# Kernel tuning notes

Measured on AMD Instinct MI355X. Metric: run time of the kernel, lower is better.

## Reference

```python
import jax, jax.numpy as jnp
import numpy as np

M, IN, H, OUT = 64, 3, 256, 3
B = 8192
W0_FIRST = 30.0
W0_HIDDEN = 30.0


def setup_inputs() -> dict:
    key = jax.random.key(0)
    ks = jax.random.split(key, 12)
    fb = 1.0 / IN                                   # first-layer bound
    hb = np.sqrt(6.0 / H) / W0_HIDDEN               # hidden bound
    x = jax.random.uniform(ks[0], (B, IN), jnp.float32, -1.0, 1.0)
    w0 = jax.random.uniform(ks[1], (M, H, IN), jnp.float32, -fb, fb)
    b0 = jnp.zeros((M, H), jnp.float32)
    w1 = jax.random.uniform(ks[2], (M, H, H), jnp.float32, -hb, hb)
    b1 = jnp.zeros((M, H), jnp.float32)
    w2 = jax.random.uniform(ks[3], (M, H, H), jnp.float32, -hb, hb)
    b2 = jnp.zeros((M, H), jnp.float32)
    w3 = jax.random.uniform(ks[4], (M, H, H), jnp.float32, -hb, hb)
    b3 = jnp.zeros((M, H), jnp.float32)
    wf = jax.random.uniform(ks[5], (M, OUT, H), jnp.float32, -hb, hb)
    bf = jnp.zeros((M, OUT), jnp.float32)
    return {"x": x, "w0": w0, "b0": b0, "w1": w1, "b1": b1,
            "w2": w2, "b2": b2, "w3": w3, "b3": b3, "wf": wf, "bf": bf}


def reference(x, w0, b0, w1, b1, w2, b2, w3, b3, wf, bf):
    # first sine layer: [B,in] x [M,H,in] -> [B,M,H]
    h = jnp.sin(W0_FIRST * (jnp.einsum('bi,moi->bmo', x, w0) + b0[None]))
    # hidden sine layers
    for w, b in ((w1, b1), (w2, b2), (w3, b3)):
        h = jnp.sin(W0_HIDDEN * (jnp.einsum('bmi,moi->bmo', h, w) + b[None]))
    # final linear: [B,M,H] x [M,out,H] -> [B,M,out]
    return jnp.einsum('bmi,moi->bmo', h, wf) + bf[None]
```

## Files before the change

kernel.cpp:

```cpp
#include <hip/hip_runtime.h>

#define BATCH 8192
#define MEXP  64
#define HDIM  256
#define INDIM 3
#define ODIM  3
#define BT    64
#define SINSC 4.774648292756860f

typedef __attribute__((ext_vector_type(8))) _Float16 f16x8;
typedef __attribute__((ext_vector_type(4))) float    f32x4;

__device__ __forceinline__ int swz(int row, int byteInRow) {
  return (row * 512 + byteInRow) ^ (((row ^ (row >> 3)) & 7) << 4);
}

__global__ void prep_hidden(const float* __restrict__ w1, const float* __restrict__ w2,
                            const float* __restrict__ w3, _Float16* __restrict__ ws) {
  int chunk = blockIdx.x * 256 + threadIdx.x;
  int lm    = chunk >> 13;
  int c     = chunk & 8191;
  int layer = lm >> 6, m = lm & 63;
  int lane  = c & 63;
  int ctks  = c >> 6;
  int ct = ctks >> 3, ks = ctks & 7;
  int col = ct * 16 + (lane & 15);
  int k   = ks * 32 + ((lane >> 4) << 3);
  const float* w = (layer == 0) ? w1 : (layer == 1) ? w2 : w3;
  const float* src = w + ((size_t)m * HDIM + col) * HDIM + k;
  f16x8 v;
#pragma unroll
  for (int j = 0; j < 8; ++j) v[j] = (_Float16)src[j];
  *(f16x8*)(ws + (size_t)chunk * 8) = v;
}

__global__ void prep_wf(const float* __restrict__ wf, _Float16* __restrict__ ws) {
  int chunk = blockIdx.x * 256 + threadIdx.x;
  int m    = chunk >> 9;
  int c    = chunk & 511;
  int lane = c & 63;
  int ks   = c >> 6;
  int col  = lane & 15;
  int k    = ks * 32 + ((lane >> 4) << 3);
  f16x8 v;
  if (col < ODIM) {
    const float* src = wf + ((size_t)m * ODIM + col) * HDIM + k;
#pragma unroll
    for (int j = 0; j < 8; ++j) v[j] = (_Float16)src[j];
  } else {
#pragma unroll
    for (int j = 0; j < 8; ++j) v[j] = (_Float16)0.0f;
  }
  *(f16x8*)(ws + (size_t)chunk * 8) = v;
}

__device__ __forceinline__ void hidden_layer(char* hb, const _Float16* __restrict__ wl,
                                             const float* __restrict__ bptr, int w, int lane) {
  f32x4 acc[4][4] = {};
#pragma unroll
  for (int ks = 0; ks < 8; ++ks) {
    f16x8 a[4];
    f16x8 bb[4];
#pragma unroll
    for (int rt = 0; rt < 4; ++rt) {
      int row = rt * 16 + (lane & 15);
      a[rt] = *(const f16x8*)(hb + swz(row, ks * 64 + ((lane >> 4) << 4)));
    }
#pragma unroll
    for (int ct = 0; ct < 4; ++ct) {
      int chunk = ((w * 4 + ct) * 8 + ks) * 64 + lane;
      bb[ct] = *(const f16x8*)(wl + chunk * 8);
    }
#pragma unroll
    for (int rt = 0; rt < 4; ++rt)
#pragma unroll
      for (int ct = 0; ct < 4; ++ct)
        acc[rt][ct] = __builtin_amdgcn_mfma_f32_16x16x32_f16(a[rt], bb[ct], acc[rt][ct], 0, 0, 0);
  }
  __syncthreads();
#pragma unroll
  for (int ct = 0; ct < 4; ++ct) {
    int col = w * 64 + ct * 16 + (lane & 15);
    float bias = bptr[col];
#pragma unroll
    for (int rt = 0; rt < 4; ++rt) {
#pragma unroll
      for (int t = 0; t < 4; ++t) {
        int row = rt * 16 + ((lane >> 4) << 2) + t;
        float h = __builtin_amdgcn_sinf((acc[rt][ct][t] + bias) * SINSC);
        *(_Float16*)(hb + swz(row, col * 2)) = (_Float16)h;
      }
    }
  }
  __syncthreads();
}

__global__ __launch_bounds__(256, 2)
void siren_fused(const float* __restrict__ x, const float* __restrict__ w0,
                 const float* __restrict__ b0, const float* __restrict__ b1,
                 const float* __restrict__ b2, const float* __restrict__ b3,
                 const float* __restrict__ bfin, const _Float16* __restrict__ wh,
                 const _Float16* __restrict__ wff, float* __restrict__ out) {
  __shared__ _Float16 hbuf[BT * HDIM];
  char* hb = (char*)hbuf;

  int tid  = threadIdx.x;
  int lane = tid & 63;
  int w    = tid >> 6;
  int id   = blockIdx.x;
  int m    = ((id & 7) << 3) + ((id >> 3) >> 7);
  int tile = (id >> 3) & 127;

  {
    int col = tid;
    const float* wp = w0 + ((size_t)m * HDIM + col) * INDIM;
    float wc0 = wp[0], wc1 = wp[1], wc2 = wp[2];
    float bc  = b0[m * HDIM + col];
    const float* xp = x + (size_t)tile * BT * INDIM;
#pragma unroll 4
    for (int r = 0; r < BT; ++r) {
      float z = fmaf(xp[r * 3 + 2], wc2, fmaf(xp[r * 3 + 1], wc1, fmaf(xp[r * 3], wc0, bc)));
      float h = __builtin_amdgcn_sinf(z * SINSC);
      *(_Float16*)(hb + swz(r, col * 2)) = (_Float16)h;
    }
  }
  __syncthreads();

  hidden_layer(hb, wh + ((size_t)0 * MEXP + m) * (HDIM * HDIM), b1 + m * HDIM, w, lane);
  hidden_layer(hb, wh + ((size_t)1 * MEXP + m) * (HDIM * HDIM), b2 + m * HDIM, w, lane);
  hidden_layer(hb, wh + ((size_t)2 * MEXP + m) * (HDIM * HDIM), b3 + m * HDIM, w, lane);

  {
    f32x4 facc = {};
    const _Float16* wfp = wff + (size_t)m * (16 * HDIM);
#pragma unroll
    for (int ks = 0; ks < 8; ++ks) {
      int row = w * 16 + (lane & 15);
      f16x8 a   = *(const f16x8*)(hb + swz(row, ks * 64 + ((lane >> 4) << 4)));
      f16x8 bfr = *(const f16x8*)(wfp + ((size_t)(ks * 64 + lane)) * 8);
      facc = __builtin_amdgcn_mfma_f32_16x16x32_f16(a, bfr, facc, 0, 0, 0);
    }
    int col = lane & 15;
    if (col < ODIM) {
      float bv = bfin[m * ODIM + col];
#pragma unroll
      for (int t = 0; t < 4; ++t) {
        int row = w * 16 + ((lane >> 4) << 2) + t;
        int b   = tile * BT + row;
        out[((size_t)b * MEXP + m) * ODIM + col] = facc[t] + bv;
      }
    }
  }
}

extern "C" void kernel_launch(void* const* d_in, const int* in_sizes, int n_in,
                              void* d_out, int out_size, void* d_ws, size_t ws_size,
                              hipStream_t stream) {
  (void)in_sizes; (void)n_in; (void)out_size; (void)ws_size;
  const float* x  = (const float*)d_in[0];
  const float* w0 = (const float*)d_in[1];
  const float* b0 = (const float*)d_in[2];
  const float* w1 = (const float*)d_in[3];
  const float* b1 = (const float*)d_in[4];
  const float* w2 = (const float*)d_in[5];
  const float* b2 = (const float*)d_in[6];
  const float* w3 = (const float*)d_in[7];
  const float* b3 = (const float*)d_in[8];
  const float* wf = (const float*)d_in[9];
  const float* bf = (const float*)d_in[10];

  _Float16* wh  = (_Float16*)d_ws;
  _Float16* wff = wh + (size_t)3 * MEXP * HDIM * HDIM;

  prep_hidden<<<6144, 256, 0, stream>>>(w1, w2, w3, wh);
  prep_wf<<<128, 256, 0, stream>>>(wf, wff);
  siren_fused<<<8192, 256, 0, stream>>>(x, w0, b0, b1, b2, b3, bf, wh, wff, (float*)d_out);
}
```

Measured before the change: 397.7 us.

## Double batch tile to 128 rows with 8 waves and swapped MFMA operands

The batch tile grows from 64 to 128 rows and each block runs 512 threads, so every block reads each expert's hidden weights for twice as many rows. Each wave now owns 32 output columns across all 8 row tiles, keeps the weight fragments in registers with a one-step prefetch, and reads activations from LDS as the B operand. The transposed accumulator layout lets each lane write four results to LDS as one vector store. The sine scale is folded into the fp16 weights during preprocessing, and the bias is applied with an fma. LDS per block doubles to 64 KB and launch bounds change to 512 threads with 4 blocks per CU, which may limit occupancy.

```diff
diff --git a/kernel.cpp b/kernel.cpp
--- a/kernel.cpp
+++ b/kernel.cpp
@@ -1,14 +1,15 @@
 #include <hip/hip_runtime.h>
 
-#define BATCH 8192
 #define MEXP  64
 #define HDIM  256
 #define INDIM 3
 #define ODIM  3
-#define BT    64
+#define BT    128
+#define NTILE 64
 #define SINSC 4.774648292756860f
 
 typedef __attribute__((ext_vector_type(8))) _Float16 f16x8;
+typedef __attribute__((ext_vector_type(4))) _Float16 f16x4;
 typedef __attribute__((ext_vector_type(4))) float    f32x4;
 
 __device__ __forceinline__ int swz(int row, int byteInRow) {
@@ -30,7 +31,7 @@
   const float* src = w + ((size_t)m * HDIM + col) * HDIM + k;
   f16x8 v;
 #pragma unroll
-  for (int j = 0; j < 8; ++j) v[j] = (_Float16)src[j];
+  for (int j = 0; j < 8; ++j) v[j] = (_Float16)(src[j] * SINSC);
   *(f16x8*)(ws + (size_t)chunk * 8) = v;
 }
 
@@ -55,47 +56,45 @@
 }
 
 __device__ __forceinline__ void hidden_layer(char* hb, const _Float16* __restrict__ wl,
-                                             const float* __restrict__ bptr, int w, int lane) {
-  f32x4 acc[4][4] = {};
+                                             const float* __restrict__ bptr,
+                                             int wid, int lane, int g) {
+  f32x4 acc[8][2] = {};
+  const f16x8* wfrag = (const f16x8*)wl;
+  int ct0 = wid * 2, ct1 = ct0 + 1;
+  f16x8 A0 = wfrag[(ct0 * 8 + 0) * 64 + lane];
+  f16x8 A1 = wfrag[(ct1 * 8 + 0) * 64 + lane];
 #pragma unroll
   for (int ks = 0; ks < 8; ++ks) {
-    f16x8 a[4];
-    f16x8 bb[4];
-#pragma unroll
-    for (int rt = 0; rt < 4; ++rt) {
-      int row = rt * 16 + (lane & 15);
-      a[rt] = *(const f16x8*)(hb + swz(row, ks * 64 + ((lane >> 4) << 4)));
+    f16x8 a0 = A0, a1 = A1;
+    if (ks < 7) {
+      A0 = wfrag[(ct0 * 8 + ks + 1) * 64 + lane];
+      A1 = wfrag[(ct1 * 8 + ks + 1) * 64 + lane];
     }
 #pragma unroll
-    for (int ct = 0; ct < 4; ++ct) {
-      int chunk = ((w * 4 + ct) * 8 + ks) * 64 + lane;
-      bb[ct] = *(const f16x8*)(wl + chunk * 8);
+    for (int rt = 0; rt < 8; ++rt) {
+      f16x8 b = *(const f16x8*)(hb + swz(rt * 16 + (lane & 15), ks * 64 + g * 16));
+      acc[rt][0] = __builtin_amdgcn_mfma_f32_16x16x32_f16(a0, b, acc[rt][0], 0, 0, 0);
+      acc[rt][1] = __builtin_amdgcn_mfma_f32_16x16x32_f16(a1, b, acc[rt][1], 0, 0, 0);
     }
-#pragma unroll
-    for (int rt = 0; rt < 4; ++rt)
-#pragma unroll
-      for (int ct = 0; ct < 4; ++ct)
-        acc[rt][ct] = __builtin_amdgcn_mfma_f32_16x16x32_f16(a[rt], bb[ct], acc[rt][ct], 0, 0, 0);
   }
   __syncthreads();
 #pragma unroll
-  for (int ct = 0; ct < 4; ++ct) {
-    int col = w * 64 + ct * 16 + (lane & 15);
-    float bias = bptr[col];
+  for (int ct = 0; ct < 2; ++ct) {
+    int c0 = wid * 32 + ct * 16 + g * 4;
+    f32x4 bias = *(const f32x4*)(bptr + c0);
 #pragma unroll
-    for (int rt = 0; rt < 4; ++rt) {
+    for (int rt = 0; rt < 8; ++rt) {
+      f16x4 v;
 #pragma unroll
-      for (int t = 0; t < 4; ++t) {
-        int row = rt * 16 + ((lane >> 4) << 2) + t;
-        float h = __builtin_amdgcn_sinf((acc[rt][ct][t] + bias) * SINSC);
-        *(_Float16*)(hb + swz(row, col * 2)) = (_Float16)h;
-      }
+      for (int t = 0; t < 4; ++t)
+        v[t] = (_Float16)__builtin_amdgcn_sinf(fmaf(bias[t], SINSC, acc[rt][ct][t]));
+      *(f16x4*)(hb + swz(rt * 16 + (lane & 15), c0 * 2)) = v;
     }
   }
   __syncthreads();
 }
 
-__global__ __launch_bounds__(256, 2)
+__global__ __launch_bounds__(512, 4)
 void siren_fused(const float* __restrict__ x, const float* __restrict__ w0,
                  const float* __restrict__ b0, const float* __restrict__ b1,
                  const float* __restrict__ b2, const float* __restrict__ b3,
@@ -106,49 +105,46 @@
 
   int tid  = threadIdx.x;
   int lane = tid & 63;
-  int w    = tid >> 6;
+  int wid  = tid >> 6;
+  int g    = lane >> 4;
   int id   = blockIdx.x;
-  int m    = ((id & 7) << 3) + ((id >> 3) >> 7);
-  int tile = (id >> 3) & 127;
+  int m    = ((id & 7) << 3) + ((id >> 3) >> 6);
+  int tile = (id >> 3) & (NTILE - 1);
 
   {
-    int col = tid;
+    int col  = tid & 255;
+    int half = tid >> 8;
     const float* wp = w0 + ((size_t)m * HDIM + col) * INDIM;
     float wc0 = wp[0], wc1 = wp[1], wc2 = wp[2];
-    float bc  = b0[m * HDIM + col];
-    const float* xp = x + (size_t)tile * BT * INDIM;
+    float bc  = b0[m * HDIM + col] * SINSC;
+    const float* xp = x + ((size_t)tile * BT + half * 64) * INDIM;
 #pragma unroll 4
-    for (int r = 0; r < BT; ++r) {
-      float z = fmaf(xp[r * 3 + 2], wc2, fmaf(xp[r * 3 + 1], wc1, fmaf(xp[r * 3], wc0, bc)));
-      float h = __builtin_amdgcn_sinf(z * SINSC);
-      *(_Float16*)(hb + swz(r, col * 2)) = (_Float16)h;
+    for (int r = 0; r < 64; ++r) {
+      float z = fmaf(xp[r * 3 + 2], wc2, fmaf(xp[r * 3 + 1], wc1, xp[r * 3] * wc0));
+      float h = __builtin_amdgcn_sinf(fmaf(z, SINSC, bc));
+      *(_Float16*)(hb + swz(half * 64 + r, col * 2)) = (_Float16)h;
     }
   }
   __syncthreads();
 
-  hidden_layer(hb, wh + ((size_t)0 * MEXP + m) * (HDIM * HDIM), b1 + m * HDIM, w, lane);
-  hidden_layer(hb, wh + ((size_t)1 * MEXP + m) * (HDIM * HDIM), b2 + m * HDIM, w, lane);
-  hidden_layer(hb, wh + ((size_t)2 * MEXP + m) * (HDIM * HDIM), b3 + m * HDIM, w, lane);
+  hidden_layer(hb, wh + ((size_t)0 * MEXP + m) * (HDIM * HDIM), b1 + m * HDIM, wid, lane, g);
+  hidden_layer(hb, wh + ((size_t)1 * MEXP + m) * (HDIM * HDIM), b2 + m * HDIM, wid, lane, g);
+  hidden_layer(hb, wh + ((size_t)2 * MEXP + m) * (HDIM * HDIM), b3 + m * HDIM, wid, lane, g);
 
   {
     f32x4 facc = {};
-    const _Float16* wfp = wff + (size_t)m * (16 * HDIM);
+    const f16x8* wfrag = (const f16x8*)(wff + (size_t)m * (16 * HDIM));
 #pragma unroll
     for (int ks = 0; ks < 8; ++ks) {
-      int row = w * 16 + (lane & 15);
-      f16x8 a   = *(const f16x8*)(hb + swz(row, ks * 64 + ((lane >> 4) << 4)));
-      f16x8 bfr = *(const f16x8*)(wfp + ((size_t)(ks * 64 + lane)) * 8);
-      facc = __builtin_amdgcn_mfma_f32_16x16x32_f16(a, bfr, facc, 0, 0, 0);
+      f16x8 b = *(const f16x8*)(hb + swz(wid * 16 + (lane & 15), ks * 64 + g * 16));
+      f16x8 a = wfrag[ks * 64 + lane];
+      facc = __builtin_amdgcn_mfma_f32_16x16x32_f16(a, b, facc, 0, 0, 0);
     }
-    int col = lane & 15;
-    if (col < ODIM) {
-      float bv = bfin[m * ODIM + col];
+    if (g == 0) {
+      size_t r = (size_t)tile * BT + wid * 16 + (lane & 15);
 #pragma unroll
-      for (int t = 0; t < 4; ++t) {
-        int row = w * 16 + ((lane >> 4) << 2) + t;
-        int b   = tile * BT + row;
-        out[((size_t)b * MEXP + m) * ODIM + col] = facc[t] + bv;
-      }
+      for (int t = 0; t < 3; ++t)
+        out[(r * MEXP + m) * ODIM + t] = facc[t] + bfin[m * ODIM + t];
     }
   }
 }
@@ -174,5 +170,5 @@
 
   prep_hidden<<<6144, 256, 0, stream>>>(w1, w2, w3, wh);
   prep_wf<<<128, 256, 0, stream>>>(wf, wff);
-  siren_fused<<<8192, 256, 0, stream>>>(x, w0, b0, b1, b2, b3, bf, wh, wff, (float*)d_out);
+  siren_fused<<<4096, 512, 0, stream>>>(x, w0, b0, b1, b2, b3, bf, wh, wff, (float*)d_out);
 }
```

After: 709.3 us. +78.3%, slower.
